# Performance work log

Measured on AMD Instinct MI355X. Metric: run time of the kernel, lower is better.

The kernel has to match this reference:

```python
import jax, jax.numpy as jnp
import numpy as np

B, T, D_IN, H, NEMB = 256, 512, 512, 512, 96


def setup_inputs() -> dict:
    key = jax.random.key(0)
    ks = jax.random.split(key, 12)
    s = 0.02
    return {
        "h": jax.random.normal(ks[0], (B, H), jnp.float32),
        "c": jax.random.normal(ks[1], (B, H), jnp.float32),
        "batch_H": jax.random.normal(ks[2], (B, T, D_IN), jnp.float32),
        "char_onehots": jax.random.uniform(ks[3], (B, NEMB), jnp.float32),
        # i2h: Linear(input_size, hidden, bias=False)
        "Wi2h": jax.random.normal(ks[4], (H, D_IN), jnp.float32) * s,
        # h2h: Linear(hidden, hidden)
        "Wh2h": jax.random.normal(ks[5], (H, H), jnp.float32) * s,
        "bh2h": jax.random.normal(ks[6], (H,), jnp.float32) * s,
        # score: Linear(hidden, 1, bias=False)
        "Wscore": jax.random.normal(ks[7], (1, H), jnp.float32) * s,
        # LSTMCell(input_size + num_embeddings, hidden); pytorch gate order i,f,g,o
        "W_ih": jax.random.normal(ks[8], (4 * H, D_IN + NEMB), jnp.float32) * s,
        "W_hh": jax.random.normal(ks[9], (4 * H, H), jnp.float32) * s,
        "b_ih": jax.random.normal(ks[10], (4 * H,), jnp.float32) * s,
        "b_hh": jax.random.normal(ks[11], (4 * H,), jnp.float32) * s,
    }


def reference(h, c, batch_H, char_onehots, Wi2h, Wh2h, bh2h, Wscore, W_ih, W_hh, b_ih, b_hh):
    # Additive (Bahdanau) attention
    batch_H_proj = jnp.einsum('btd,hd->bth', batch_H, Wi2h)        # [B,T,H]
    prev_hidden_proj = h @ Wh2h.T + bh2h                            # [B,H]
    e = jnp.einsum('bth,oh->bto', jnp.tanh(batch_H_proj + prev_hidden_proj[:, None, :]), Wscore)  # [B,T,1]
    alpha = jax.nn.softmax(e, axis=1)                               # [B,T,1]
    context = jnp.einsum('bt,btd->bd', alpha[..., 0], batch_H)      # [B,D_IN]
    x = jnp.concatenate([context, char_onehots], axis=1)            # [B, D_IN+NEMB]
    # dropout in eval mode = identity (deterministic reference)
    # LSTMCell step (pytorch gate order: i, f, g, o)
    gates = x @ W_ih.T + b_ih + h @ W_hh.T + b_hh                   # [B,4H]
    i_g, f_g, g_g, o_g = jnp.split(gates, 4, axis=1)
    i_g = jax.nn.sigmoid(i_g)
    f_g = jax.nn.sigmoid(f_g)
    g_g = jnp.tanh(g_g)
    o_g = jax.nn.sigmoid(o_g)
    c_new = f_g * c + i_g * g_g
    h_new = o_g * jnp.tanh(c_new)
    return h_new, c_new, alpha
```

## Files before the change

### kernel.cpp

```cpp
#include <hip/hip_runtime.h>
#include <stdint.h>

#define B_    256
#define T_    512
#define DIN   512
#define H_    512
#define NEMB_ 96
#define BT    131072
#define KG    1120

typedef __attribute__((ext_vector_type(8))) short short8;
typedef __attribute__((ext_vector_type(4))) float f32x4;
typedef __attribute__((ext_vector_type(16))) float f32x16;

__device__ __forceinline__ unsigned bf16_rne(float f) {
    unsigned u = __float_as_uint(f);
    return (u + 0x7FFF + ((u >> 16) & 1)) >> 16;
}
__device__ __forceinline__ unsigned pack2(float a, float b) {
    return bf16_rne(a) | (bf16_rne(b) << 16);
}
__device__ __forceinline__ float tanh_fast(float x) {
    float ex = __expf(2.f * x);
    return 1.f - 2.f / (ex + 1.f);
}
__device__ __forceinline__ float sigmoid_fast(float x) {
    return 1.f / (1.f + __expf(-x));
}

__global__ void k_cvt(const float* __restrict__ W, unsigned* __restrict__ Wb) {
    int i = blockIdx.x * 256 + threadIdx.x;
    float2 f = ((const float2*)W)[i];
    Wb[i] = pack2(f.x, f.y);
}

__global__ void k_prevproj(const float* __restrict__ hin, const float* __restrict__ Whh,
                           const float* __restrict__ bh, float* __restrict__ pp) {
    __shared__ float hs[512];
    int b = blockIdx.x >> 4, tc = blockIdx.x & 15;
    int tid = threadIdx.x;
    hs[tid]       = hin[b * 512 + tid];
    hs[256 + tid] = hin[b * 512 + 256 + tid];
    __syncthreads();
    int wave = tid >> 6, lane = tid & 63;
    int o = lane >> 3, kg = lane & 7;
    int t = tc * 32 + wave * 8 + o;
    const float4* wr = (const float4*)(Whh + (size_t)t * 512);
    const float4* hv = (const float4*)hs;
    float acc = 0.f;
#pragma unroll
    for (int j = 0; j < 16; ++j) {
        float4 w = wr[j * 8 + kg];
        float4 x = hv[j * 8 + kg];
        acc += w.x * x.x + w.y * x.y + w.z * x.z + w.w * x.w;
    }
#pragma unroll
    for (int off = 1; off < 8; off <<= 1) acc += __shfl_xor(acc, off, 8);
    if (kg == 0) pp[b * 512 + t] = acc + bh[t];
}

__launch_bounds__(512, 4)
__global__ void k_scores(const float* __restrict__ A,
                         const unsigned short* __restrict__ Wb,
                         const float* __restrict__ pp,
                         const float* __restrict__ wsc,
                         float* __restrict__ e)
{
    __shared__ uint4 ldsA[4096];
    __shared__ float es[64];
    int tid = threadIdx.x;
    int blockRow = blockIdx.x * 64;
    int b = blockRow >> 9;
    int lane = tid & 63, wave = tid >> 6;
    int l31 = lane & 31, lh = lane >> 5, l7 = lane & 7;

    if (tid < 64) es[tid] = 0.f;

    const float4* A4 = (const float4*)A;
#pragma unroll
    for (int it = 0; it < 8; ++it) {
        int row = it * 8 + wave;
        size_t gidx = (size_t)(blockRow + row) * 128 + (size_t)lane * 2;
        float4 f0 = A4[gidx], f1 = A4[gidx + 1];
        uint4 u;
        u.x = pack2(f0.x, f0.y); u.y = pack2(f0.z, f0.w);
        u.z = pack2(f1.x, f1.y); u.w = pack2(f1.z, f1.w);
        ldsA[row * 64 + (lane ^ (row & 7))] = u;
    }
    __syncthreads();

    const short8* lds8 = (const short8*)ldsA;
    int base0 = l31 * 64;
    int base1 = (32 + l31) * 64;

    int n0 = wave * 64 + l31;
    const short8* b0p = (const short8*)(Wb + (size_t)n0 * 512);
    const short8* b1p = (const short8*)(Wb + (size_t)(n0 + 32) * 512);
    f32x16 acc00 = {0.f}, acc01 = {0.f}, acc10 = {0.f}, acc11 = {0.f};
#pragma unroll
    for (int c = 0; c < 32; ++c) {
        int g = c * 2 + lh;
        int gx = g ^ l7;
        short8 a0 = lds8[base0 + gx];
        short8 a1 = lds8[base1 + gx];
        short8 b0 = b0p[g];
        short8 b1 = b1p[g];
        acc00 = __builtin_amdgcn_mfma_f32_32x32x16_bf16(a0, b0, acc00, 0, 0, 0);
        acc10 = __builtin_amdgcn_mfma_f32_32x32x16_bf16(a1, b0, acc10, 0, 0, 0);
        acc01 = __builtin_amdgcn_mfma_f32_32x32x16_bf16(a0, b1, acc01, 0, 0, 0);
        acc11 = __builtin_amdgcn_mfma_f32_32x32x16_bf16(a1, b1, acc11, 0, 0, 0);
    }

    float pp0 = pp[b * 512 + n0],      ws0 = wsc[n0];
    float pp1 = pp[b * 512 + n0 + 32], ws1 = wsc[n0 + 32];
#pragma unroll
    for (int r = 0; r < 16; ++r) {
        float v0 = tanh_fast(acc00[r] + pp0) * ws0 + tanh_fast(acc01[r] + pp1) * ws1;
        float v1 = tanh_fast(acc10[r] + pp0) * ws0 + tanh_fast(acc11[r] + pp1) * ws1;
#pragma unroll
        for (int off = 1; off < 32; off <<= 1) {
            v0 += __shfl_xor(v0, off, 32);
            v1 += __shfl_xor(v1, off, 32);
        }
        if (l31 == 0) {
            int row = lh * 4 + (r & 3) + 8 * (r >> 2);
            atomicAdd(&es[row],      v0);
            atomicAdd(&es[32 + row], v1);
        }
    }
    __syncthreads();
    if (tid < 64) e[blockRow + tid] = es[tid];
}

__global__ void k_softmax(float* __restrict__ ealpha) {
    __shared__ float red[8];
    int b = blockIdx.x, tid = threadIdx.x;
    float v0 = ealpha[b * 512 + tid];
    float v1 = ealpha[b * 512 + 256 + tid];
    float mx = fmaxf(v0, v1);
    for (int off = 32; off; off >>= 1) mx = fmaxf(mx, __shfl_xor(mx, off, 64));
    if ((tid & 63) == 0) red[tid >> 6] = mx;
    __syncthreads();
    mx = fmaxf(fmaxf(red[0], red[1]), fmaxf(red[2], red[3]));
    float x0 = __expf(v0 - mx), x1 = __expf(v1 - mx);
    float s = x0 + x1;
    for (int off = 32; off; off >>= 1) s += __shfl_xor(s, off, 64);
    if ((tid & 63) == 0) red[4 + (tid >> 6)] = s;
    __syncthreads();
    s = red[4] + red[5] + red[6] + red[7];
    float inv = 1.f / s;
    ealpha[b * 512 + tid]       = x0 * inv;
    ealpha[b * 512 + 256 + tid] = x1 * inv;
}

__global__ void k_context(const float* __restrict__ A, const float* __restrict__ alpha,
                          float* __restrict__ ctx) {
    int b = blockIdx.x >> 3, chunk = blockIdx.x & 7;
    int tid = threadIdx.x;
    const float2* A2 = (const float2*)A;
    float ax = 0.f, ay = 0.f;
    int t0 = chunk * 64;
    for (int t = 0; t < 64; ++t) {
        float a = alpha[b * 512 + t0 + t];
        float2 v = A2[(size_t)(b * 512 + t0 + t) * 256 + tid];
        ax += a * v.x; ay += a * v.y;
    }
    atomicAdd(&ctx[b * 512 + tid * 2],     ax);
    atomicAdd(&ctx[b * 512 + tid * 2 + 1], ay);
}

__global__ void k_xcat(const float* __restrict__ ctx, const float* __restrict__ oneh,
                       const float* __restrict__ hin, unsigned short* __restrict__ xb) {
    int b = blockIdx.x, tid = threadIdx.x;
    for (int k = tid; k < KG; k += 256) {
        float v;
        if (k < 512)      v = ctx[b * 512 + k];
        else if (k < 608) v = oneh[b * 96 + (k - 512)];
        else              v = hin[b * 512 + (k - 608)];
        xb[(size_t)b * KG + k] = (unsigned short)bf16_rne(v);
    }
}

__global__ void k_wcat(const float* __restrict__ Wih, const float* __restrict__ Whh,
                       unsigned short* __restrict__ Wg) {
    int g = blockIdx.x, tid = threadIdx.x;
    for (int k = tid; k < KG; k += 256) {
        float v;
        if (k < 608) v = Wih[(size_t)g * 608 + k];
        else         v = Whh[(size_t)g * 512 + (k - 608)];
        Wg[(size_t)g * KG + k] = (unsigned short)bf16_rne(v);
    }
}

__launch_bounds__(256, 4)
__global__ void k_gates(const unsigned short* __restrict__ xb,
                        const unsigned short* __restrict__ Wg,
                        float* __restrict__ gates5) {
    int tid = threadIdx.x;
    int lane = tid & 63, wave = tid >> 6;
    int l31 = lane & 31, lh = lane >> 5;
    int wid = blockIdx.x * 4 + wave;
    int gI = wid & 63, bI = (wid >> 6) & 7, kI = wid >> 9;

    const short8* ax = (const short8*)xb + (size_t)(bI * 32 + l31) * 140 + kI * 28;
    const short8* bx = (const short8*)Wg + (size_t)(gI * 32 + l31) * 140 + kI * 28;

    f32x16 acc = {0.f};
#pragma unroll
    for (int c = 0; c < 14; ++c) {
        short8 a = ax[c * 2 + lh];
        short8 b = bx[c * 2 + lh];
        acc = __builtin_amdgcn_mfma_f32_32x32x16_bf16(a, b, acc, 0, 0, 0);
    }
    float* gout = gates5 + (size_t)kI * (B_ * 2048)
                + (size_t)(bI * 32 + 4 * lh) * 2048 + gI * 32 + l31;
#pragma unroll
    for (int r = 0; r < 16; ++r)
        gout[(size_t)((r & 3) + 8 * (r >> 2)) * 2048] = acc[r];
}

__global__ void k_lstm(const float* __restrict__ gates5, const float* __restrict__ c,
                       const float* __restrict__ bih, const float* __restrict__ bhh,
                       float* __restrict__ out) {
    int i = blockIdx.x * 256 + threadIdx.x;
    int b = i >> 9, u = i & 511;
    size_t base = (size_t)b * 2048 + u;
    float gi = bih[u]        + bhh[u];
    float gf = bih[512 + u]  + bhh[512 + u];
    float gg = bih[1024 + u] + bhh[1024 + u];
    float go = bih[1536 + u] + bhh[1536 + u];
#pragma unroll
    for (int s = 0; s < 5; ++s) {
        const float* g = gates5 + (size_t)s * (B_ * 2048) + base;
        gi += g[0]; gf += g[512]; gg += g[1024]; go += g[1536];
    }
    float si = sigmoid_fast(gi);
    float sf = sigmoid_fast(gf);
    float tg = tanh_fast(gg);
    float so = sigmoid_fast(go);
    float cn = sf * c[i] + si * tg;
    float hn = so * tanh_fast(cn);
    out[i] = hn;
    out[BT + i] = cn;
}

extern "C" void kernel_launch(void* const* d_in, const int* in_sizes, int n_in,
                              void* d_out, int out_size, void* d_ws, size_t ws_size,
                              hipStream_t stream) {
    const float* hin  = (const float*)d_in[0];
    const float* c    = (const float*)d_in[1];
    const float* bH   = (const float*)d_in[2];
    const float* oneh = (const float*)d_in[3];
    const float* Wi2h = (const float*)d_in[4];
    const float* Wh2h = (const float*)d_in[5];
    const float* bh2h = (const float*)d_in[6];
    const float* Wsc  = (const float*)d_in[7];
    const float* Wih  = (const float*)d_in[8];
    const float* Whh  = (const float*)d_in[9];
    const float* bih  = (const float*)d_in[10];
    const float* bhh  = (const float*)d_in[11];
    float* out = (float*)d_out;
    float* alpha = out + 2 * BT;

    char* w = (char*)d_ws;
    unsigned* Wb          = (unsigned*)w;
    float* pp             = (float*)(w + 524288);
    float* ctx            = (float*)(w + 1048576);
    unsigned short* xb    = (unsigned short*)(w + 1572864);
    unsigned short* Wg    = (unsigned short*)(w + 2146304);
    float* gates5         = (float*)(w + 6733824);

    hipMemsetAsync(ctx, 0, 524288, stream);
    k_cvt     <<<512, 256, 0, stream>>>(Wi2h, Wb);
    k_wcat    <<<2048, 256, 0, stream>>>(Wih, Whh, Wg);
    k_prevproj<<<4096, 256, 0, stream>>>(hin, Wh2h, bh2h, pp);
    k_scores  <<<2048, 512, 0, stream>>>(bH, (const unsigned short*)Wb, pp, Wsc, alpha);
    k_softmax <<<256, 256, 0, stream>>>(alpha);
    k_context <<<2048, 256, 0, stream>>>(bH, alpha, ctx);
    k_xcat    <<<256, 256, 0, stream>>>(ctx, oneh, hin, xb);
    k_gates   <<<640, 256, 0, stream>>>(xb, Wg, gates5);
    k_lstm    <<<512, 256, 0, stream>>>(gates5, c, bih, bhh, out);
}
```

Before: 571.6 us.

## Pre-swizzle bf16 weight and input operands into MFMA fragment order; restructure context reduction

Weight and activation conversion kernels now write bf16 data directly in per-lane MFMA fragment order, so the score and gate GEMMs load B/A operands with contiguous coalesced 16-byte accesses instead of strided row reads. The context kernel is restructured to one block per batch half with an LDS reduction across waves, removing the memset and global atomics. Conversion kernels use vectorized 8-element packing. This adds index arithmetic in the conversion kernels.

```diff
diff --git a/kernel.cpp b/kernel.cpp
--- a/kernel.cpp
+++ b/kernel.cpp
@@ -20,6 +20,12 @@
 __device__ __forceinline__ unsigned pack2(float a, float b) {
     return bf16_rne(a) | (bf16_rne(b) << 16);
 }
+__device__ __forceinline__ uint4 pack8(float4 f0, float4 f1) {
+    uint4 u;
+    u.x = pack2(f0.x, f0.y); u.y = pack2(f0.z, f0.w);
+    u.z = pack2(f1.x, f1.y); u.w = pack2(f1.z, f1.w);
+    return u;
+}
 __device__ __forceinline__ float tanh_fast(float x) {
     float ex = __expf(2.f * x);
     return 1.f - 2.f / (ex + 1.f);
@@ -28,10 +34,13 @@
     return 1.f / (1.f + __expf(-x));
 }
 
-__global__ void k_cvt(const float* __restrict__ W, unsigned* __restrict__ Wb) {
-    int i = blockIdx.x * 256 + threadIdx.x;
-    float2 f = ((const float2*)W)[i];
-    Wb[i] = pack2(f.x, f.y);
+__global__ void k_bswz(const float* __restrict__ W, uint4* __restrict__ Wbf) {
+    int u = blockIdx.x * 256 + threadIdx.x;
+    int l = u & 63, c = (u >> 6) & 31, nt = u >> 11;
+    int row = nt * 32 + (l & 31);
+    int k0 = (c * 2 + (l >> 5)) * 8;
+    const float4* W4 = (const float4*)(W + (size_t)row * 512 + k0);
+    Wbf[u] = pack8(W4[0], W4[1]);
 }
 
 __global__ void k_prevproj(const float* __restrict__ hin, const float* __restrict__ Whh,
@@ -61,7 +70,7 @@
 
 __launch_bounds__(512, 4)
 __global__ void k_scores(const float* __restrict__ A,
-                         const unsigned short* __restrict__ Wb,
+                         const uint4* __restrict__ Wbf,
                          const float* __restrict__ pp,
                          const float* __restrict__ wsc,
                          float* __restrict__ e)
@@ -82,10 +91,7 @@
         int row = it * 8 + wave;
         size_t gidx = (size_t)(blockRow + row) * 128 + (size_t)lane * 2;
         float4 f0 = A4[gidx], f1 = A4[gidx + 1];
-        uint4 u;
-        u.x = pack2(f0.x, f0.y); u.y = pack2(f0.z, f0.w);
-        u.z = pack2(f1.x, f1.y); u.w = pack2(f1.z, f1.w);
-        ldsA[row * 64 + (lane ^ (row & 7))] = u;
+        ldsA[row * 64 + (lane ^ (row & 7))] = pack8(f0, f1);
     }
     __syncthreads();
 
@@ -93,9 +99,7 @@
     int base0 = l31 * 64;
     int base1 = (32 + l31) * 64;
 
-    int n0 = wave * 64 + l31;
-    const short8* b0p = (const short8*)(Wb + (size_t)n0 * 512);
-    const short8* b1p = (const short8*)(Wb + (size_t)(n0 + 32) * 512);
+    const short8* wf = (const short8*)Wbf + wave * 4096 + lane;
     f32x16 acc00 = {0.f}, acc01 = {0.f}, acc10 = {0.f}, acc11 = {0.f};
 #pragma unroll
     for (int c = 0; c < 32; ++c) {
@@ -103,14 +107,15 @@
         int gx = g ^ l7;
         short8 a0 = lds8[base0 + gx];
         short8 a1 = lds8[base1 + gx];
-        short8 b0 = b0p[g];
-        short8 b1 = b1p[g];
+        short8 b0 = wf[c * 64];
+        short8 b1 = wf[2048 + c * 64];
         acc00 = __builtin_amdgcn_mfma_f32_32x32x16_bf16(a0, b0, acc00, 0, 0, 0);
         acc10 = __builtin_amdgcn_mfma_f32_32x32x16_bf16(a1, b0, acc10, 0, 0, 0);
         acc01 = __builtin_amdgcn_mfma_f32_32x32x16_bf16(a0, b1, acc01, 0, 0, 0);
         acc11 = __builtin_amdgcn_mfma_f32_32x32x16_bf16(a1, b1, acc11, 0, 0, 0);
     }
 
+    int n0 = wave * 64 + l31;
     float pp0 = pp[b * 512 + n0],      ws0 = wsc[n0];
     float pp1 = pp[b * 512 + n0 + 32], ws1 = wsc[n0 + 32];
 #pragma unroll
@@ -155,46 +160,62 @@
 
 __global__ void k_context(const float* __restrict__ A, const float* __restrict__ alpha,
                           float* __restrict__ ctx) {
-    int b = blockIdx.x >> 3, chunk = blockIdx.x & 7;
-    int tid = threadIdx.x;
-    const float2* A2 = (const float2*)A;
-    float ax = 0.f, ay = 0.f;
-    int t0 = chunk * 64;
-    for (int t = 0; t < 64; ++t) {
-        float a = alpha[b * 512 + t0 + t];
-        float2 v = A2[(size_t)(b * 512 + t0 + t) * 256 + tid];
-        ax += a * v.x; ay += a * v.y;
-    }
-    atomicAdd(&ctx[b * 512 + tid * 2],     ax);
-    atomicAdd(&ctx[b * 512 + tid * 2 + 1], ay);
+    __shared__ float4 part[4][64];
+    int b = blockIdx.x >> 1, half = blockIdx.x & 1;
+    int tid = threadIdx.x, wave = tid >> 6, lane = tid & 63;
+    const float4* A4 = (const float4*)A;
+    const float* al = alpha + b * 512;
+    size_t rbase = (size_t)b * 512;
+    float4 acc = {0.f, 0.f, 0.f, 0.f};
+#pragma unroll 8
+    for (int t = wave; t < 512; t += 4) {
+        float a = al[t];
+        float4 v = A4[(rbase + t) * 128 + half * 64 + lane];
+        acc.x += a * v.x; acc.y += a * v.y; acc.z += a * v.z; acc.w += a * v.w;
+    }
+    part[wave][lane] = acc;
+    __syncthreads();
+    if (tid < 64) {
+        float4 p0 = part[0][tid], p1 = part[1][tid], p2 = part[2][tid], p3 = part[3][tid];
+        float4 r;
+        r.x = p0.x + p1.x + p2.x + p3.x;
+        r.y = p0.y + p1.y + p2.y + p3.y;
+        r.z = p0.z + p1.z + p2.z + p3.z;
+        r.w = p0.w + p1.w + p2.w + p3.w;
+        ((float4*)ctx)[b * 128 + half * 64 + tid] = r;
+    }
 }
 
 __global__ void k_xcat(const float* __restrict__ ctx, const float* __restrict__ oneh,
-                       const float* __restrict__ hin, unsigned short* __restrict__ xb) {
-    int b = blockIdx.x, tid = threadIdx.x;
-    for (int k = tid; k < KG; k += 256) {
-        float v;
-        if (k < 512)      v = ctx[b * 512 + k];
-        else if (k < 608) v = oneh[b * 96 + (k - 512)];
-        else              v = hin[b * 512 + (k - 608)];
-        xb[(size_t)b * KG + k] = (unsigned short)bf16_rne(v);
-    }
+                       const float* __restrict__ hin, uint4* __restrict__ xbf) {
+    int u = blockIdx.x * 256 + threadIdx.x;
+    int l = u & 63, r = u >> 6;
+    int c = r % 70, bt = r / 70;
+    int row = bt * 32 + (l & 31);
+    int k0 = (c * 2 + (l >> 5)) * 8;
+    const float4* s4;
+    if (k0 < 512)      s4 = (const float4*)(ctx  + (size_t)row * 512 + k0);
+    else if (k0 < 608) s4 = (const float4*)(oneh + (size_t)row * 96  + (k0 - 512));
+    else               s4 = (const float4*)(hin  + (size_t)row * 512 + (k0 - 608));
+    xbf[u] = pack8(s4[0], s4[1]);
 }
 
 __global__ void k_wcat(const float* __restrict__ Wih, const float* __restrict__ Whh,
-                       unsigned short* __restrict__ Wg) {
-    int g = blockIdx.x, tid = threadIdx.x;
-    for (int k = tid; k < KG; k += 256) {
-        float v;
-        if (k < 608) v = Wih[(size_t)g * 608 + k];
-        else         v = Whh[(size_t)g * 512 + (k - 608)];
-        Wg[(size_t)g * KG + k] = (unsigned short)bf16_rne(v);
-    }
+                       uint4* __restrict__ wgf) {
+    int u = blockIdx.x * 256 + threadIdx.x;
+    int l = u & 63, r = u >> 6;
+    int c = r % 70, gt = r / 70;
+    int g = gt * 32 + (l & 31);
+    int k0 = (c * 2 + (l >> 5)) * 8;
+    const float4* s4;
+    if (k0 < 608) s4 = (const float4*)(Wih + (size_t)g * 608 + k0);
+    else          s4 = (const float4*)(Whh + (size_t)g * 512 + (k0 - 608));
+    wgf[u] = pack8(s4[0], s4[1]);
 }
 
 __launch_bounds__(256, 4)
-__global__ void k_gates(const unsigned short* __restrict__ xb,
-                        const unsigned short* __restrict__ Wg,
+__global__ void k_gates(const uint4* __restrict__ xbf,
+                        const uint4* __restrict__ wgf,
                         float* __restrict__ gates5) {
     int tid = threadIdx.x;
     int lane = tid & 63, wave = tid >> 6;
@@ -202,14 +223,14 @@
     int wid = blockIdx.x * 4 + wave;
     int gI = wid & 63, bI = (wid >> 6) & 7, kI = wid >> 9;
 
-    const short8* ax = (const short8*)xb + (size_t)(bI * 32 + l31) * 140 + kI * 28;
-    const short8* bx = (const short8*)Wg + (size_t)(gI * 32 + l31) * 140 + kI * 28;
+    const short8* ax = (const short8*)xbf + (size_t)(bI * 70 + kI * 14) * 64 + lane;
+    const short8* bx = (const short8*)wgf + (size_t)(gI * 70 + kI * 14) * 64 + lane;
 
     f32x16 acc = {0.f};
 #pragma unroll
     for (int c = 0; c < 14; ++c) {
-        short8 a = ax[c * 2 + lh];
-        short8 b = bx[c * 2 + lh];
+        short8 a = ax[c * 64];
+        short8 b = bx[c * 64];
         acc = __builtin_amdgcn_mfma_f32_32x32x16_bf16(a, b, acc, 0, 0, 0);
     }
     float* gout = gates5 + (size_t)kI * (B_ * 2048)
@@ -263,21 +284,20 @@
     float* alpha = out + 2 * BT;
 
     char* w = (char*)d_ws;
-    unsigned* Wb          = (unsigned*)w;
-    float* pp             = (float*)(w + 524288);
-    float* ctx            = (float*)(w + 1048576);
-    unsigned short* xb    = (unsigned short*)(w + 1572864);
-    unsigned short* Wg    = (unsigned short*)(w + 2146304);
-    float* gates5         = (float*)(w + 6733824);
-
-    hipMemsetAsync(ctx, 0, 524288, stream);
-    k_cvt     <<<512, 256, 0, stream>>>(Wi2h, Wb);
-    k_wcat    <<<2048, 256, 0, stream>>>(Wih, Whh, Wg);
+    uint4* Wbf    = (uint4*)w;
+    float* pp     = (float*)(w + 524288);
+    float* ctx    = (float*)(w + 1048576);
+    uint4* xbf    = (uint4*)(w + 1572864);
+    uint4* wgf    = (uint4*)(w + 2146304);
+    float* gates5 = (float*)(w + 6733824);
+
+    k_bswz    <<<128, 256, 0, stream>>>(Wi2h, Wbf);
+    k_wcat    <<<1120, 256, 0, stream>>>(Wih, Whh, wgf);
     k_prevproj<<<4096, 256, 0, stream>>>(hin, Wh2h, bh2h, pp);
-    k_scores  <<<2048, 512, 0, stream>>>(bH, (const unsigned short*)Wb, pp, Wsc, alpha);
+    k_scores  <<<2048, 512, 0, stream>>>(bH, Wbf, pp, Wsc, alpha);
     k_softmax <<<256, 256, 0, stream>>>(alpha);
-    k_context <<<2048, 256, 0, stream>>>(bH, alpha, ctx);
-    k_xcat    <<<256, 256, 0, stream>>>(ctx, oneh, hin, xb);
-    k_gates   <<<640, 256, 0, stream>>>(xb, Wg, gates5);
+    k_context <<<512, 256, 0, stream>>>(bH, alpha, ctx);
+    k_xcat    <<<140, 256, 0, stream>>>(ctx, oneh, hin, xbf);
+    k_gates   <<<640, 256, 0, stream>>>(xbf, wgf, gates5);
     k_lstm    <<<512, 256, 0, stream>>>(gates5, c, bih, bhh, out);
 }
```

Result: faster. 527.0 us (-7.8%).
